# Performance work log

Measured on AMD Instinct MI355X. Metric: run time of the kernel, lower is better.

Reference implementation:

```python
import jax, jax.numpy as jnp
import numpy as np
from jax import lax

NUM_CLASSES = 80
SCALE_XY = 1.0
NMS_THRESH = 0.7
SCORE_THRESH = 0.05
OBJ_THRESH = 0.5
MAX_DETS = 100  # fixed top-K candidate pool fed to NMS (jit-friendly padding)


def setup_inputs() -> dict:
    key = jax.random.key(0)
    k1, k2 = jax.random.split(key)
    x = jax.random.normal(k1, (16, 255, 128, 128), dtype=jnp.float32)
    anchors = jax.random.uniform(k2, (3, 2), dtype=jnp.float32, minval=0.05, maxval=0.7)
    return {"x": x, "anchors": anchors}


def decode(x, anchors):
    # x: [b, A*(5+C), h, w] -> boxes [b,h,w,A,4], obj [b,h,w,A], scores [b,h,w,A,C]
    b, _, h, w = x.shape
    A = anchors.shape[0]
    out = x.reshape(b, A, 5 + NUM_CLASSES, h, w).transpose(0, 3, 4, 1, 2)
    c_x = jnp.arange(w, dtype=jnp.float32).reshape(1, 1, w, 1)
    c_y = jnp.arange(h, dtype=jnp.float32).reshape(1, h, 1, 1)
    b_xy = SCALE_XY * jax.nn.sigmoid(out[..., :2]) - 0.5 * (SCALE_XY - 1.0)
    b_x = (b_xy[..., 0] + c_x) / w
    b_y = (b_xy[..., 1] + c_y) / h
    b_wh = jnp.clip(jnp.exp(out[..., 2:4]) * anchors.reshape(1, 1, 1, A, 2), 0.0, 2.0)
    top_left = jnp.stack([b_x, b_y], axis=-1) - 0.5 * b_wh
    boxes = jnp.concatenate([top_left, top_left + b_wh], axis=-1)
    return boxes, out[..., 4], out[..., 5:]


def box_iou(a, b):
    # a: [N,4], b: [M,4] in (x1,y1,x2,y2)
    area_a = jnp.clip(a[:, 2] - a[:, 0], 0) * jnp.clip(a[:, 3] - a[:, 1], 0)
    area_b = jnp.clip(b[:, 2] - b[:, 0], 0) * jnp.clip(b[:, 3] - b[:, 1], 0)
    lt = jnp.maximum(a[:, None, :2], b[None, :, :2])
    rb = jnp.minimum(a[:, None, 2:], b[None, :, 2:])
    wh = jnp.clip(rb - lt, 0)
    inter = wh[..., 0] * wh[..., 1]
    union = area_a[:, None] + area_b[None, :] - inter
    return inter / jnp.maximum(union, 1e-12)


def greedy_nms(iou, valid):
    # boxes assumed sorted by descending score; valid: [K] bool
    K = iou.shape[0]
    idx = jnp.arange(K)

    def body(i, keep):
        # if box i is kept, suppress later boxes overlapping it too much
        sup = keep[i] & (iou[i] > NMS_THRESH) & (idx > i)
        return keep & ~sup

    return lax.fori_loop(0, K, body, valid)


def _per_image(boxes, b_o, b_scores):
    # boxes [h,w,A,4], b_o [h,w,A], b_scores [h,w,A,C]
    boxes = jnp.clip(boxes.reshape(-1, 4), 0.0, 1.0)
    obj = jax.nn.sigmoid(b_o.reshape(-1))
    cls = jax.nn.sigmoid(b_scores.reshape(-1, NUM_CLASSES))
    cls_score = cls.max(axis=-1)
    labels = jnp.argmax(cls, axis=-1)
    scores = cls_score * obj
    valid = (obj >= OBJ_THRESH) & (scores >= SCORE_THRESH)
    masked = jnp.where(valid, scores, -1.0)
    top_s, top_i = lax.top_k(masked, MAX_DETS)
    top_boxes = boxes[top_i]
    top_labels = labels[top_i]
    cand = top_s > 0.0
    keep = greedy_nms(box_iou(top_boxes, top_boxes), cand)
    out_boxes = jnp.where(keep[:, None], top_boxes, 0.0)
    out_scores = jnp.where(keep, top_s, 0.0)
    out_labels = jnp.where(keep, top_labels, -1)
    return out_boxes, out_scores, out_labels, keep


def reference(x, anchors):
    boxes, b_o, b_scores = decode(x, anchors)
    # fixed-size padded detections per image (equivalent to post_process with
    # dynamic lists, padded to MAX_DETS; keep mask marks valid rows)
    return jax.vmap(_per_image)(boxes, b_o, b_scores)
```

## Files before the change

### kernel.cpp

```cpp
#include <hip/hip_runtime.h>
#include <math.h>

#define B 16
#define A 3
#define W 128
#define HW 16384
#define NCH 255
#define NCLS 80
#define NCAND 49152
#define K 100
#define NBINS 4096
#define CAP 1024

__device__ __forceinline__ float sigmoidf_(float v) {
    return 1.0f / (1.0f + expf(-v));
}

__device__ __forceinline__ bool pair_before(float sa, int ia, float sb, int ib) {
    return (sa > sb) || (sa == sb && ia < ib);
}

__global__ __launch_bounds__(256) void k_scores(const float* __restrict__ x,
                                                float* __restrict__ scores,
                                                unsigned char* __restrict__ labels) {
    int t = blockIdx.x * 256 + threadIdx.x;
    int b = t / (A * HW / 4);
    int r = t - b * (A * HW / 4);
    int a = r / (HW / 4);
    int q = r - a * (HW / 4);
    int hw = q * 4;
    const float* base = x + (size_t)(b * NCH + a * 85) * HW + hw;

    float4 o4 = *(const float4*)(base + 4 * HW);
    float4 m4 = *(const float4*)(base + 5 * HW);
    int amx = 0, amy = 0, amz = 0, amw = 0;
    #pragma unroll
    for (int c = 1; c < NCLS; ++c) {
        float4 v = *(const float4*)(base + (5 + c) * HW);
        bool gx = v.x > m4.x; amx = gx ? c : amx; m4.x = gx ? v.x : m4.x;
        bool gy = v.y > m4.y; amy = gy ? c : amy; m4.y = gy ? v.y : m4.y;
        bool gz = v.z > m4.z; amz = gz ? c : amz; m4.z = gz ? v.z : m4.z;
        bool gw = v.w > m4.w; amw = gw ? c : amw; m4.w = gw ? v.w : m4.w;
    }
    float ol[4] = {o4.x, o4.y, o4.z, o4.w};
    float ml[4] = {m4.x, m4.y, m4.z, m4.w};
    float outv[4];
    #pragma unroll
    for (int l = 0; l < 4; ++l) {
        float obj = sigmoidf_(ol[l]);
        float cls = sigmoidf_(ml[l]);
        float sc = obj * cls;
        bool valid = (obj >= 0.5f) && (sc >= 0.05f);
        outv[l] = valid ? sc : -1.0f;
    }
    size_t off = (size_t)b * NCAND + a * HW + hw;
    *(float4*)(scores + off) = make_float4(outv[0], outv[1], outv[2], outv[3]);
    *(uchar4*)(labels + off) = make_uchar4((unsigned char)amx, (unsigned char)amy,
                                           (unsigned char)amz, (unsigned char)amw);
}

__global__ __launch_bounds__(1024) void k_final3(const float* __restrict__ x,
                                                 const float* __restrict__ anchors,
                                                 const float* __restrict__ scores,
                                                 const unsigned char* __restrict__ labels,
                                                 float* __restrict__ out) {
    __shared__ unsigned int hist[NBINS];
    __shared__ unsigned int suf[1024];
    __shared__ int tstar, sh_thr;
    __shared__ unsigned int sh_cnt;
    __shared__ float cs[CAP];
    __shared__ int ci[CAP];
    __shared__ float ts[K];
    __shared__ int tix[K];
    __shared__ float bx[K][4];
    __shared__ float area[K];
    __shared__ int lab[K];
    __shared__ unsigned int sup[K][4];
    __shared__ unsigned int keepw[4];

    int b = blockIdx.x;
    int tid = threadIdx.x;
    const float* sb = scores + (size_t)b * NCAND;

    for (int i = tid; i < NBINS; i += 1024) hist[i] = 0;
    if (tid == 0) { tstar = -1; sh_thr = 0; sh_cnt = 0; }
    if (tid < 4) keepw[tid] = 0u;
    for (int i = tid; i < K * 4; i += 1024) ((unsigned int*)sup)[i] = 0u;
    if (tid < K) { ts[tid] = -3.0f; tix[tid] = 0x7FFFFFFF; }
    __syncthreads();

    #pragma unroll
    for (int it = 0; it < 12; ++it) {
        int o = (it * 1024 + tid) * 4;
        float4 v = *(const float4*)(sb + o);
        float sv[4] = {v.x, v.y, v.z, v.w};
        #pragma unroll
        for (int l = 0; l < 4; ++l) {
            float s = sv[l];
            if (s > 0.0f) {
                int bin = (int)(s * (float)NBINS);
                bin = bin > NBINS - 1 ? NBINS - 1 : bin;
                atomicAdd(&hist[bin], 1u);
            }
        }
    }
    __syncthreads();

    unsigned int acc = hist[tid * 4] + hist[tid * 4 + 1] +
                       hist[tid * 4 + 2] + hist[tid * 4 + 3];
    suf[tid] = acc;
    __syncthreads();
    for (int off = 1; off < 1024; off <<= 1) {
        unsigned int add = (tid + off < 1024) ? suf[tid + off] : 0u;
        __syncthreads();
        suf[tid] += add;
        __syncthreads();
    }
    if (suf[tid] >= K && (tid == 1023 || suf[tid + 1] < K)) tstar = tid;
    __syncthreads();
    if (tid == 0 && tstar >= 0) {
        int t = tstar;
        unsigned int running = (t < 1023) ? suf[t + 1] : 0u;
        int result = t * 4;
        for (int bin = t * 4 + 3; bin >= t * 4; --bin) {
            running += hist[bin];
            if (running >= K) { result = bin; break; }
        }
        sh_thr = result;
    }
    __syncthreads();

    int thr = sh_thr;
    #pragma unroll
    for (int it = 0; it < 12; ++it) {
        int o = (it * 1024 + tid) * 4;
        float4 v = *(const float4*)(sb + o);
        float sv[4] = {v.x, v.y, v.z, v.w};
        #pragma unroll
        for (int l = 0; l < 4; ++l) {
            float s = sv[l];
            if (s > 0.0f && (int)(s * (float)NBINS) >= thr) {
                unsigned int p = atomicAdd(&sh_cnt, 1u);
                if (p < CAP) {
                    int so = o + l;
                    int aa = so >> 14;
                    int hh = so & (HW - 1);
                    cs[p] = s;
                    ci[p] = hh * A + aa;
                }
            }
        }
    }
    __syncthreads();
    int n = (int)sh_cnt; if (n > CAP) n = CAP;

    if (tid < n) {
        float s0 = cs[tid]; int i0 = ci[tid];
        int rank = 0;
        for (int j = 0; j < n; ++j)
            rank += pair_before(cs[j], ci[j], s0, i0) ? 1 : 0;
        if (rank < K) { ts[rank] = s0; tix[rank] = i0; }
    }
    __syncthreads();

    if (tid < K && ts[tid] > 0.0f) {
        int nidx = tix[tid];
        int a = nidx % A;
        int hw = nidx / A;
        int cx = hw % W;
        int cy = hw / W;
        const float* base = x + (size_t)(b * NCH + a * 85) * HW + hw;
        float tx = base[0];
        float ty = base[HW];
        float tw = base[2 * HW];
        float th = base[3 * HW];
        float bcx = (sigmoidf_(tx) + (float)cx) / 128.0f;
        float bcy = (sigmoidf_(ty) + (float)cy) / 128.0f;
        float bw = fminf(fmaxf(expf(tw) * anchors[a * 2 + 0], 0.0f), 2.0f);
        float bh = fminf(fmaxf(expf(th) * anchors[a * 2 + 1], 0.0f), 2.0f);
        float x1 = bcx - 0.5f * bw;
        float y1 = bcy - 0.5f * bh;
        float x2 = x1 + bw;
        float y2 = y1 + bh;
        x1 = fminf(fmaxf(x1, 0.0f), 1.0f);
        y1 = fminf(fmaxf(y1, 0.0f), 1.0f);
        x2 = fminf(fmaxf(x2, 0.0f), 1.0f);
        y2 = fminf(fmaxf(y2, 0.0f), 1.0f);
        bx[tid][0] = x1; bx[tid][1] = y1; bx[tid][2] = x2; bx[tid][3] = y2;
        area[tid] = fmaxf(x2 - x1, 0.0f) * fmaxf(y2 - y1, 0.0f);
        lab[tid] = (int)labels[(size_t)b * NCAND + a * HW + hw];
        atomicOr(&keepw[tid >> 5], 1u << (tid & 31));
    }
    __syncthreads();

    for (int p = tid; p < K * K; p += 1024) {
        int i = p / K, j = p % K;
        if (j > i && ts[i] > 0.0f && ts[j] > 0.0f) {
            float lx = fmaxf(bx[i][0], bx[j][0]);
            float ly = fmaxf(bx[i][1], bx[j][1]);
            float rx = fminf(bx[i][2], bx[j][2]);
            float ry = fminf(bx[i][3], bx[j][3]);
            float iw = fmaxf(rx - lx, 0.0f);
            float ih = fmaxf(ry - ly, 0.0f);
            float inter = iw * ih;
            float uni = area[i] + area[j] - inter;
            float iou = inter / fmaxf(uni, 1e-12f);
            if (iou > 0.7f) atomicOr(&sup[i][j >> 5], 1u << (j & 31));
        }
    }
    __syncthreads();

    if (tid == 0) {
        unsigned int kw0 = keepw[0], kw1 = keepw[1], kw2 = keepw[2], kw3 = keepw[3];
        for (int i = 0; i < K; ++i) {
            unsigned int kwi = (i < 32) ? kw0 : (i < 64) ? kw1 : (i < 96) ? kw2 : kw3;
            if ((kwi >> (i & 31)) & 1u) {
                kw0 &= ~sup[i][0];
                kw1 &= ~sup[i][1];
                kw2 &= ~sup[i][2];
                kw3 &= ~sup[i][3];
            }
        }
        keepw[0] = kw0; keepw[1] = kw1; keepw[2] = kw2; keepw[3] = kw3;
    }
    __syncthreads();

    if (tid < K) {
        int kp = (keepw[tid >> 5] >> (tid & 31)) & 1u;
        float sc = ts[tid];
        float* ob = out + (size_t)b * K * 4;
        float* osc = out + (size_t)B * K * 4;
        float* olab = osc + (size_t)B * K;
        float* okp = olab + (size_t)B * K;
        ob[tid * 4 + 0] = kp ? bx[tid][0] : 0.0f;
        ob[tid * 4 + 1] = kp ? bx[tid][1] : 0.0f;
        ob[tid * 4 + 2] = kp ? bx[tid][2] : 0.0f;
        ob[tid * 4 + 3] = kp ? bx[tid][3] : 0.0f;
        osc[b * K + tid] = kp ? sc : 0.0f;
        olab[b * K + tid] = kp ? (float)lab[tid] : -1.0f;
        okp[b * K + tid] = kp ? 1.0f : 0.0f;
    }
}

extern "C" void kernel_launch(void* const* d_in, const int* in_sizes, int n_in,
                              void* d_out, int out_size, void* d_ws, size_t ws_size,
                              hipStream_t stream) {
    const float* x = (const float*)d_in[0];
    const float* anchors = (const float*)d_in[1];
    float* out = (float*)d_out;

    float* scores = (float*)d_ws;
    unsigned char* labels = (unsigned char*)(scores + (size_t)B * NCAND);

    k_scores<<<(B * A * HW / 4) / 256, 256, 0, stream>>>(x, scores, labels);
    k_final3<<<B, 1024, 0, stream>>>(x, anchors, scores, labels, out);
}
```

Measured before the change: 70.75 us.

## Build score histogram in scoring kernel via global atomics, simplify threshold search

Moves the per-image score histogram out of the single-block-per-image tail kernel into the massively parallel scoring kernel, using global atomics on a zeroed workspace histogram. The tail kernel then only copies the histogram into LDS and finds the top-K threshold with one wavefront using shuffles and a ballot, in place of a 1024-thread block scan. The goal is to remove the serialized pass over 49K scores per image that ran on only 16 blocks. In exchange it adds a memset launch and contended global atomics, which are limited to valid candidates.

```diff
diff --git a/kernel.cpp b/kernel.cpp
--- a/kernel.cpp
+++ b/kernel.cpp
@@ -22,7 +22,8 @@
 
 __global__ __launch_bounds__(256) void k_scores(const float* __restrict__ x,
                                                 float* __restrict__ scores,
-                                                unsigned char* __restrict__ labels) {
+                                                unsigned char* __restrict__ labels,
+                                                unsigned int* __restrict__ hist) {
     int t = blockIdx.x * 256 + threadIdx.x;
     int b = t / (A * HW / 4);
     int r = t - b * (A * HW / 4);
@@ -45,13 +46,20 @@
     float ol[4] = {o4.x, o4.y, o4.z, o4.w};
     float ml[4] = {m4.x, m4.y, m4.z, m4.w};
     float outv[4];
+    unsigned int* hb = hist + b * NBINS;
     #pragma unroll
     for (int l = 0; l < 4; ++l) {
         float obj = sigmoidf_(ol[l]);
         float cls = sigmoidf_(ml[l]);
         float sc = obj * cls;
         bool valid = (obj >= 0.5f) && (sc >= 0.05f);
-        outv[l] = valid ? sc : -1.0f;
+        float ms = valid ? sc : -1.0f;
+        outv[l] = ms;
+        if (ms > 0.0f) {
+            int bin = (int)(ms * (float)NBINS);
+            bin = bin > NBINS - 1 ? NBINS - 1 : bin;
+            atomicAdd(&hb[bin], 1u);
+        }
     }
     size_t off = (size_t)b * NCAND + a * HW + hw;
     *(float4*)(scores + off) = make_float4(outv[0], outv[1], outv[2], outv[3]);
@@ -59,14 +67,14 @@
                                            (unsigned char)amz, (unsigned char)amw);
 }
 
-__global__ __launch_bounds__(1024) void k_final3(const float* __restrict__ x,
-                                                 const float* __restrict__ anchors,
-                                                 const float* __restrict__ scores,
-                                                 const unsigned char* __restrict__ labels,
-                                                 float* __restrict__ out) {
-    __shared__ unsigned int hist[NBINS];
-    __shared__ unsigned int suf[1024];
-    __shared__ int tstar, sh_thr;
+__global__ __launch_bounds__(1024) void k_tail(const float* __restrict__ x,
+                                               const float* __restrict__ anchors,
+                                               const float* __restrict__ scores,
+                                               const unsigned char* __restrict__ labels,
+                                               const unsigned int* __restrict__ hist,
+                                               float* __restrict__ out) {
+    __shared__ unsigned int lh[NBINS];
+    __shared__ int sh_thr;
     __shared__ unsigned int sh_cnt;
     __shared__ float cs[CAP];
     __shared__ int ci[CAP];
@@ -82,51 +90,38 @@
     int tid = threadIdx.x;
     const float* sb = scores + (size_t)b * NCAND;
 
-    for (int i = tid; i < NBINS; i += 1024) hist[i] = 0;
-    if (tid == 0) { tstar = -1; sh_thr = 0; sh_cnt = 0; }
+    for (int i = tid; i < NBINS; i += 1024) lh[i] = hist[b * NBINS + i];
+    if (tid == 0) { sh_thr = 0; sh_cnt = 0; }
     if (tid < 4) keepw[tid] = 0u;
     for (int i = tid; i < K * 4; i += 1024) ((unsigned int*)sup)[i] = 0u;
     if (tid < K) { ts[tid] = -3.0f; tix[tid] = 0x7FFFFFFF; }
     __syncthreads();
 
-    #pragma unroll
-    for (int it = 0; it < 12; ++it) {
-        int o = (it * 1024 + tid) * 4;
-        float4 v = *(const float4*)(sb + o);
-        float sv[4] = {v.x, v.y, v.z, v.w};
+    if (tid < 64) {
+        unsigned int c = 0;
         #pragma unroll
-        for (int l = 0; l < 4; ++l) {
-            float s = sv[l];
-            if (s > 0.0f) {
-                int bin = (int)(s * (float)NBINS);
-                bin = bin > NBINS - 1 ? NBINS - 1 : bin;
-                atomicAdd(&hist[bin], 1u);
+        for (int j = 0; j < 64; ++j)
+            c += lh[tid * 64 + ((j + tid) & 63)];
+        unsigned int s = c;
+        #pragma unroll
+        for (int off = 1; off < 64; off <<= 1) {
+            unsigned int v = __shfl_down(s, off);
+            if (tid + off < 64) s += v;
+        }
+        unsigned long long mask = __ballot(s >= K);
+        int lstar = -1;
+        if (mask) lstar = 63 - __clzll(mask);
+        unsigned int snext = 0;
+        if (lstar >= 0 && lstar < 63) snext = (unsigned int)__shfl((int)s, lstar + 1);
+        if (lstar >= 0 && tid == lstar) {
+            unsigned int running = snext;
+            int result = lstar * 64;
+            for (int bin = lstar * 64 + 63; bin >= lstar * 64; --bin) {
+                running += lh[bin];
+                if (running >= K) { result = bin; break; }
             }
-        }
-    }
-    __syncthreads();
-
-    unsigned int acc = hist[tid * 4] + hist[tid * 4 + 1] +
-                       hist[tid * 4 + 2] + hist[tid * 4 + 3];
-    suf[tid] = acc;
-    __syncthreads();
-    for (int off = 1; off < 1024; off <<= 1) {
-        unsigned int add = (tid + off < 1024) ? suf[tid + off] : 0u;
-        __syncthreads();
-        suf[tid] += add;
-        __syncthreads();
-    }
-    if (suf[tid] >= K && (tid == 1023 || suf[tid + 1] < K)) tstar = tid;
-    __syncthreads();
-    if (tid == 0 && tstar >= 0) {
-        int t = tstar;
-        unsigned int running = (t < 1023) ? suf[t + 1] : 0u;
-        int result = t * 4;
-        for (int bin = t * 4 + 3; bin >= t * 4; --bin) {
-            running += hist[bin];
-            if (running >= K) { result = bin; break; }
-        }
-        sh_thr = result;
+            sh_thr = result;
+        }
     }
     __syncthreads();
 
@@ -251,7 +246,9 @@
 
     float* scores = (float*)d_ws;
     unsigned char* labels = (unsigned char*)(scores + (size_t)B * NCAND);
-
-    k_scores<<<(B * A * HW / 4) / 256, 256, 0, stream>>>(x, scores, labels);
-    k_final3<<<B, 1024, 0, stream>>>(x, anchors, scores, labels, out);
-}
+    unsigned int* hist = (unsigned int*)(labels + (size_t)B * NCAND);
+
+    hipMemsetAsync(hist, 0, (size_t)B * NBINS * sizeof(unsigned int), stream);
+    k_scores<<<(B * A * HW / 4) / 256, 256, 0, stream>>>(x, scores, labels, hist);
+    k_tail<<<B, 1024, 0, stream>>>(x, anchors, scores, labels, hist, out);
+}
```

Measured after the change: 114.5 us. 1.62x slower.
